# Kernel tuning notes

Measured on AMD Instinct MI355X. Metric: run time of the kernel, lower is better.

Reference implementation:

```python
import jax, jax.numpy as jnp
import numpy as np

N_DRUG = 20000
N_DIS = 20000
E = 300000
D_IN = 128
D_OUT = 128
W_SCALE = 0.05  # ~xavier-ish scale so leaky_relu/softmax stay well-conditioned


def setup_inputs() -> dict:
    key = jax.random.key(0)
    ks = jax.random.split(key, 17)
    f32 = jnp.float32
    inp = {
        'feat_drug': jax.random.normal(ks[0], (N_DRUG, D_IN), dtype=f32),
        'feat_disease': jax.random.normal(ks[1], (N_DIS, D_IN), dtype=f32),
        'W_ind': jax.random.normal(ks[2], (D_IN, D_OUT), dtype=f32) * W_SCALE,
        'b_ind': jax.random.normal(ks[3], (D_OUT,), dtype=f32) * W_SCALE,
        'a_ind': jax.random.normal(ks[4], (2 * D_OUT,), dtype=f32) * W_SCALE,
        'W_rev': jax.random.normal(ks[5], (D_IN, D_OUT), dtype=f32) * W_SCALE,
        'b_rev': jax.random.normal(ks[6], (D_OUT,), dtype=f32) * W_SCALE,
        'a_rev': jax.random.normal(ks[7], (2 * D_OUT,), dtype=f32) * W_SCALE,
        'W_dd': jax.random.normal(ks[8], (D_IN, D_OUT), dtype=f32) * W_SCALE,
        'b_dd': jax.random.normal(ks[9], (D_OUT,), dtype=f32) * W_SCALE,
        'a_dd': jax.random.normal(ks[10], (2 * D_OUT,), dtype=f32) * W_SCALE,
        'src_ind': jax.random.randint(ks[11], (E,), 0, N_DRUG, dtype=jnp.int32),
        'dst_ind': jax.random.randint(ks[12], (E,), 0, N_DIS, dtype=jnp.int32),
        'src_rev': jax.random.randint(ks[13], (E,), 0, N_DIS, dtype=jnp.int32),
        'dst_rev': jax.random.randint(ks[14], (E,), 0, N_DRUG, dtype=jnp.int32),
        'src_dd': jax.random.randint(ks[15], (E,), 0, N_DIS, dtype=jnp.int32),
        'dst_dd': jax.random.randint(ks[16], (E,), 0, N_DIS, dtype=jnp.int32),
    }
    return inp


def segment_softmax(e, seg, num_segments):
    # numerically stable softmax over variable-degree neighborhoods (dst segments)
    m = jax.ops.segment_max(e, seg, num_segments=num_segments)
    p = jnp.exp(e - m[seg])
    s = jax.ops.segment_sum(p, seg, num_segments=num_segments)
    return p / s[seg]


def _etype_agg(Wh_src, Wh_dst_key, a, src, dst, n_dst):
    # attn_fc(cat([Wh_src[src], Wh_dst_key[dst]])) decomposed into per-node
    # scalar projections, then gathered per edge (same math, far less traffic)
    d = Wh_src.shape[1]
    el = Wh_src @ a[:d]        # [n_src]
    er = Wh_dst_key @ a[d:]    # [n_dst]
    e = jax.nn.leaky_relu(el[src] + er[dst])          # [E], slope 0.01 as in torch
    alpha = segment_softmax(e, dst, n_dst)            # per-dst softmax (DGL mailbox)
    msg = alpha[:, None] * Wh_src[src]                # [E, d]
    return jax.ops.segment_sum(msg, dst, num_segments=n_dst)


def reference(feat_drug, feat_disease, W_ind, b_ind, a_ind, W_rev, b_rev, a_rev,
              W_dd, b_dd, a_dd, src_ind, dst_ind, src_rev, dst_rev, src_dd, dst_dd):
    # per-etype linear on source node type
    Wh_ind = feat_drug @ W_ind + b_ind       # drug nodes, etype 'indication'
    Wh_rev = feat_disease @ W_rev + b_rev    # disease nodes, etype 'rev_indication'
    Wh_dd = feat_disease @ W_dd + b_dd       # disease nodes, etype 'disease_disease'
    n_drug = feat_drug.shape[0]
    n_dis = feat_disease.shape[0]
    # etype 'indication' (drug->disease): dst key is Wh_rev_indication
    h_dis_ind = _etype_agg(Wh_ind, Wh_rev, a_ind, src_ind, dst_ind, n_dis)
    # etype 'rev_indication' (disease->drug): dst key is Wh_indication
    h_drug = _etype_agg(Wh_rev, Wh_ind, a_rev, src_rev, dst_rev, n_drug)
    # etype 'disease_disease' (homotypic): both keys Wh_dd
    h_dis_dd = _etype_agg(Wh_dd, Wh_dd, a_dd, src_dd, dst_dd, n_dis)
    # multi_update_all(..., 'sum'): sum per-etype reductions per dst node type
    h_disease = h_dis_ind + h_dis_dd
    return h_drug, h_disease
```

## Files before the change

### kernel.cpp

```cpp
#include <hip/hip_runtime.h>
#include <hip/hip_bf16.h>

typedef __hip_bfloat16 bf16;
typedef __attribute__((ext_vector_type(8))) short bf16x8;
typedef __attribute__((ext_vector_type(4))) float f32x4;

#define N_NODE 20000
#define D      128
#define NEDGE  300000
#define NROW   (3 * N_NODE)
#define NBIN   ((NROW + 255) >> 8)
#define NB3    220
#define CHUNK  4096
#define GBE    ((N_NODE + 63) / 64)
#define GEMMB  (3 * GBE)
#define WT_LD  132

__device__ __forceinline__ short f2bs(float x) {
    bf16 h = __float2bfloat16(x);
    short s; __builtin_memcpy(&s, &h, 2); return s;
}

union SharedA {
    short Wt[D * WT_LD];
    int   h[NBIN];
};

__global__ __launch_bounds__(256) void gemm_and_count(
    const float* __restrict__ feat_drug, const float* __restrict__ feat_dis,
    const float* __restrict__ W_ind, const float* __restrict__ b_ind,
    const float* __restrict__ a_ind,
    const float* __restrict__ W_rev, const float* __restrict__ b_rev,
    const float* __restrict__ a_rev,
    const float* __restrict__ W_dd, const float* __restrict__ b_dd,
    const float* __restrict__ a_dd,
    const int* __restrict__ dst_rev, const int* __restrict__ dst_ind,
    const int* __restrict__ dst_dd,
    bf16* __restrict__ Wh_all, float* __restrict__ el_all,
    float* __restrict__ er_all, int* __restrict__ bin_part) {
    __shared__ SharedA su;
    const int tid = threadIdx.x;

    if (blockIdx.x >= GEMMB) {
        const int blk = blockIdx.x - GEMMB;
        for (int i = tid; i < NBIN; i += 256) su.h[i] = 0;
        __syncthreads();
        const int base = blk * CHUNK;
        const int lim = min(base + CHUNK, 3 * NEDGE);
        for (int i = base + tid; i < lim; i += 256) {
            const int t = (i >= 2 * NEDGE) ? 2 : (i >= NEDGE ? 1 : 0);
            const int e = i - t * NEDGE;
            const int d = (t == 0 ? dst_rev : (t == 1 ? dst_ind : dst_dd))[e];
            atomicAdd(&su.h[(t * N_NODE + d) >> 8], 1);
        }
        __syncthreads();
        for (int i = tid; i < NBIN; i += 256)
            bin_part[blk * NBIN + i] = su.h[i];
        return;
    }

    const int t  = blockIdx.x / GBE;
    const int mb = blockIdx.x - t * GBE;

    const float *feat, *W, *bias, *va, *vb;
    float *el_o, *er_o;
    if (t == 0)      { feat = feat_dis;  W = W_rev; bias = b_rev; va = a_rev; vb = a_ind + D; el_o = el_all;              er_o = er_all + N_NODE; }
    else if (t == 1) { feat = feat_drug; W = W_ind; bias = b_ind; va = a_ind; vb = a_rev + D; el_o = el_all + N_NODE;     er_o = er_all; }
    else             { feat = feat_dis;  W = W_dd;  bias = b_dd;  va = a_dd;  vb = a_dd + D;  el_o = el_all + 2 * N_NODE; er_o = er_all + 2 * N_NODE; }
    bf16* wh_o = Wh_all + (size_t)t * N_NODE * D;

    for (int i = tid * 4; i < D * D; i += 1024) {
        const float4 wv = *(const float4*)(W + i);
        const int k = i >> 7, n = i & (D - 1);
        su.Wt[(n + 0) * WT_LD + k] = f2bs(wv.x);
        su.Wt[(n + 1) * WT_LD + k] = f2bs(wv.y);
        su.Wt[(n + 2) * WT_LD + k] = f2bs(wv.z);
        su.Wt[(n + 3) * WT_LD + k] = f2bs(wv.w);
    }
    __syncthreads();

    const int wave = tid >> 6, lane = tid & 63;
    const int q = lane >> 4, nn = lane & 15;
    const int row0 = mb * 64 + wave * 16;
    const int arow = min(row0 + nn, N_NODE - 1);

    f32x4 acc[8];
#pragma unroll
    for (int nt = 0; nt < 8; ++nt) acc[nt] = (f32x4){0.f, 0.f, 0.f, 0.f};

#pragma unroll
    for (int ks = 0; ks < 4; ++ks) {
        const float* ap = feat + (size_t)arow * D + ks * 32 + q * 8;
        const float4 fa = *(const float4*)ap;
        const float4 fb = *(const float4*)(ap + 4);
        bf16x8 afrag;
        afrag[0] = f2bs(fa.x); afrag[1] = f2bs(fa.y);
        afrag[2] = f2bs(fa.z); afrag[3] = f2bs(fa.w);
        afrag[4] = f2bs(fb.x); afrag[5] = f2bs(fb.y);
        afrag[6] = f2bs(fb.z); afrag[7] = f2bs(fb.w);
#pragma unroll
        for (int nt = 0; nt < 8; ++nt) {
            const bf16x8 bfrag =
                *(const bf16x8*)(&su.Wt[(nt * 16 + nn) * WT_LD + ks * 32 + q * 8]);
            acc[nt] = __builtin_amdgcn_mfma_f32_16x16x32_bf16(afrag, bfrag,
                                                              acc[nt], 0, 0, 0);
        }
    }

    float biasv[8], vav[8], vbv[8];
#pragma unroll
    for (int nt = 0; nt < 8; ++nt) {
        const int col = nt * 16 + nn;
        biasv[nt] = bias[col]; vav[nt] = va[col]; vbv[nt] = vb[col];
    }
    float pel[4] = {0.f, 0.f, 0.f, 0.f};
    float per_[4] = {0.f, 0.f, 0.f, 0.f};
    short* whs = (short*)wh_o;
#pragma unroll
    for (int nt = 0; nt < 8; ++nt) {
#pragma unroll
        for (int r = 0; r < 4; ++r) {
            const float c = acc[nt][r] + biasv[nt];
            const int grow = row0 + q * 4 + r;
            if (grow < N_NODE)
                whs[(size_t)grow * D + nt * 16 + nn] = f2bs(c);
            pel[r] = fmaf(c, vav[nt], pel[r]);
            per_[r] = fmaf(c, vbv[nt], per_[r]);
        }
    }
#pragma unroll
    for (int r = 0; r < 4; ++r) {
#pragma unroll
        for (int mask = 1; mask < 16; mask <<= 1) {
            pel[r]  += __shfl_xor(pel[r],  mask, 64);
            per_[r] += __shfl_xor(per_[r], mask, 64);
        }
        const int grow = row0 + q * 4 + r;
        if (nn == 0 && grow < N_NODE) {
            el_o[grow] = pel[r];
            er_o[grow] = per_[r];
        }
    }
}

__global__ __launch_bounds__(256) void binscat(
    const int* __restrict__ src_rev, const int* __restrict__ dst_rev,
    const int* __restrict__ src_ind, const int* __restrict__ dst_ind,
    const int* __restrict__ src_dd,  const int* __restrict__ dst_dd,
    const int* __restrict__ bin_part, int* __restrict__ bin_base_g,
    int* __restrict__ row_ptr, unsigned* __restrict__ bin_buf) {
    __shared__ int runc[NBIN];
    __shared__ int wsum[4];
    const int blk = blockIdx.x;
    const int tid = threadIdx.x;
    const int lane = tid & 63, wave = tid >> 6;

    int tot = 0, pre = 0;
    if (tid < NBIN) {
        for (int j = 0; j < NB3; ++j) {
            const int c = bin_part[j * NBIN + tid];
            tot += c;
            pre += (j < blk) ? c : 0;
        }
    }
    int v = (tid < NBIN) ? tot : 0;
    const int orig = v;
#pragma unroll
    for (int off = 1; off < 64; off <<= 1) {
        int t = __shfl_up(v, off, 64);
        if (lane >= off) v += t;
    }
    if (lane == 63) wsum[wave] = v;
    __syncthreads();
    if (tid == 0) {
        int a = 0;
#pragma unroll
        for (int w = 0; w < 4; ++w) { int t = wsum[w]; wsum[w] = a; a += t; }
    }
    __syncthreads();
    const int excl = wsum[wave] + v - orig;
    if (tid < NBIN) runc[tid] = excl + pre;
    if (blk == 0) {
        if (tid < NBIN) bin_base_g[tid] = excl;
        if (tid == 0) { bin_base_g[NBIN] = 3 * NEDGE; row_ptr[NROW] = 3 * NEDGE; }
    }
    __syncthreads();

    const int base = blk * CHUNK;
    const int lim = min(base + CHUNK, 3 * NEDGE);
    for (int i = base + tid; i < lim; i += 256) {
        const int t = (i >= 2 * NEDGE) ? 2 : (i >= NEDGE ? 1 : 0);
        const int e = i - t * NEDGE;
        const int sl = (t == 0 ? src_rev : (t == 1 ? src_ind : src_dd))[e];
        const int dl = (t == 0 ? dst_rev : (t == 1 ? dst_ind : dst_dd))[e];
        const int row = t * N_NODE + dl;
        const int slot = atomicAdd(&runc[row >> 8], 1);
        bin_buf[slot] = ((unsigned)row << 16) | (unsigned)(t * N_NODE + sl);
    }
}

__global__ __launch_bounds__(256) void binsort(
    const int* __restrict__ bin_base, const unsigned* __restrict__ bin_buf,
    int* __restrict__ row_ptr, unsigned short* __restrict__ edge_src16) {
    __shared__ int rowcnt[256];
    __shared__ int rankc[256];
    __shared__ int wsum[4];
    const int b = blockIdx.x;
    const int tid = threadIdx.x;
    const int beg = bin_base[b], end = bin_base[b + 1];
    rowcnt[tid] = 0;
    __syncthreads();
    for (int i = beg + tid; i < end; i += 256)
        atomicAdd(&rowcnt[(bin_buf[i] >> 16) & 255], 1);
    __syncthreads();
    const int lane = tid & 63, wave = tid >> 6;
    int v = rowcnt[tid];
    const int orig = v;
#pragma unroll
    for (int off = 1; off < 64; off <<= 1) {
        int t = __shfl_up(v, off, 64);
        if (lane >= off) v += t;
    }
    if (lane == 63) wsum[wave] = v;
    __syncthreads();
    if (tid == 0) {
        int a = 0;
#pragma unroll
        for (int w = 0; w < 4; ++w) { int t = wsum[w]; wsum[w] = a; a += t; }
    }
    __syncthreads();
    const int excl = wsum[wave] + v - orig;
    const int row = b * 256 + tid;
    if (row < NROW) row_ptr[row] = beg + excl;
    rankc[tid] = beg + excl;
    __syncthreads();
    for (int i = beg + tid; i < end; i += 256) {
        const unsigned u = bin_buf[i];
        const int slot = atomicAdd(&rankc[(u >> 16) & 255], 1);
        edge_src16[slot] = (unsigned short)(u & 0xFFFFu);
    }
}

__device__ __forceinline__ void process_chunk(
    int msrc, float mpe, int m, float inv, int sub, int fl,
    const bf16* __restrict__ Wh_all, float* __restrict__ acc) {
#pragma unroll 2
    for (int t = 0; t < m; t += 4) {
        const int   s = __shfl(msrc, t + sub, 64);
        const float c = __shfl(mpe,  t + sub, 64) * inv;
        const uint4 u = ((const uint4*)(Wh_all + (size_t)s * D))[fl];
        acc[0] = fmaf(c, __uint_as_float(u.x << 16),          acc[0]);
        acc[1] = fmaf(c, __uint_as_float(u.x & 0xFFFF0000u),  acc[1]);
        acc[2] = fmaf(c, __uint_as_float(u.y << 16),          acc[2]);
        acc[3] = fmaf(c, __uint_as_float(u.y & 0xFFFF0000u),  acc[3]);
        acc[4] = fmaf(c, __uint_as_float(u.z << 16),          acc[4]);
        acc[5] = fmaf(c, __uint_as_float(u.z & 0xFFFF0000u),  acc[5]);
        acc[6] = fmaf(c, __uint_as_float(u.w << 16),          acc[6]);
        acc[7] = fmaf(c, __uint_as_float(u.w & 0xFFFF0000u),  acc[7]);
    }
}

__device__ __forceinline__ void do_range(
    const unsigned short* __restrict__ edge_src16,
    const float* __restrict__ el_all, float er_r,
    const bf16* __restrict__ Wh_all,
    int beg, int end, int lane, int sub, int fl, float* __restrict__ acc) {
    if (end <= beg) return;
    const int deg = end - beg;
    const int m0 = min(deg, 64);

    int msrc0 = 0; float mpe0 = 0.f;
    if (lane < m0) {
        msrc0 = edge_src16[beg + lane];
        float v = el_all[msrc0] + er_r;
        v = v > 0.f ? v : 0.01f * v;
        mpe0 = __expf(v);
    }
    float ssum = mpe0;
    for (int base = beg + 64; base < end; base += 64) {
        const int m = min(end - base, 64);
        if (lane < m) {
            const int sr = edge_src16[base + lane];
            float v = el_all[sr] + er_r;
            v = v > 0.f ? v : 0.01f * v;
            ssum += __expf(v);
        }
    }
#pragma unroll
    for (int off = 32; off > 0; off >>= 1) ssum += __shfl_down(ssum, off, 64);
    const float inv = 1.0f / __shfl(ssum, 0, 64);

    process_chunk(msrc0, mpe0, m0, inv, sub, fl, Wh_all, acc);
    for (int base = beg + 64; base < end; base += 64) {
        const int m = min(end - base, 64);
        int msrc = 0; float mpe = 0.f;
        if (lane < m) {
            msrc = edge_src16[base + lane];
            float v = el_all[msrc] + er_r;
            v = v > 0.f ? v : 0.01f * v;
            mpe = __expf(v);
        }
        process_chunk(msrc, mpe, m, inv, sub, fl, Wh_all, acc);
    }
}

__global__ __launch_bounds__(256) void gather_all(
    const int* __restrict__ row_ptr, const unsigned short* __restrict__ edge_src16,
    const float* __restrict__ el_all, const float* __restrict__ er_all,
    const bf16* __restrict__ Wh_all, float* __restrict__ out) {
    const int w = blockIdx.x * (blockDim.x >> 6) + (threadIdx.x >> 6);
    const int lane = threadIdx.x & 63;
    if (w >= 2 * N_NODE) return;
    const int sub = lane >> 4, fl = lane & 15;

    float acc[8];
#pragma unroll
    for (int j = 0; j < 8; ++j) acc[j] = 0.f;

    do_range(edge_src16, el_all, er_all[w], Wh_all,
             row_ptr[w], row_ptr[w + 1], lane, sub, fl, acc);
    if (w >= N_NODE) {
        const int r = w + N_NODE;
        do_range(edge_src16, el_all, er_all[r], Wh_all,
                 row_ptr[r], row_ptr[r + 1], lane, sub, fl, acc);
    }

#pragma unroll
    for (int j = 0; j < 8; ++j) {
        acc[j] += __shfl_xor(acc[j], 16, 64);
        acc[j] += __shfl_xor(acc[j], 32, 64);
    }
    if (sub == 0) {
        float4* orow = (float4*)(out + (size_t)w * D);
        orow[2 * fl]     = make_float4(acc[0], acc[1], acc[2], acc[3]);
        orow[2 * fl + 1] = make_float4(acc[4], acc[5], acc[6], acc[7]);
    }
}

extern "C" void kernel_launch(void* const* d_in, const int* in_sizes, int n_in,
                              void* d_out, int out_size, void* d_ws, size_t ws_size,
                              hipStream_t stream) {
    const float* feat_drug    = (const float*)d_in[0];
    const float* feat_disease = (const float*)d_in[1];
    const float* W_ind = (const float*)d_in[2];
    const float* b_ind = (const float*)d_in[3];
    const float* a_ind = (const float*)d_in[4];
    const float* W_rev = (const float*)d_in[5];
    const float* b_rev = (const float*)d_in[6];
    const float* a_rev = (const float*)d_in[7];
    const float* W_dd  = (const float*)d_in[8];
    const float* b_dd  = (const float*)d_in[9];
    const float* a_dd  = (const float*)d_in[10];
    const int* src_ind = (const int*)d_in[11];
    const int* dst_ind = (const int*)d_in[12];
    const int* src_rev = (const int*)d_in[13];
    const int* dst_rev = (const int*)d_in[14];
    const int* src_dd  = (const int*)d_in[15];
    const int* dst_dd  = (const int*)d_in[16];
    float* out = (float*)d_out;
    (void)in_sizes; (void)n_in; (void)out_size; (void)ws_size;

    char* w = (char*)d_ws;
    bf16*  Wh_all   = (bf16*)w;
    float* el_all   = (float*)(w + 15360000);
    float* er_all   = (float*)(w + 15600000);
    int*   row_ptr  = (int*)(w + 15840000);
    int*   bin_base = (int*)(w + 16080032);
    int*   bin_part = (int*)(w + 16081056);
    unsigned* bin_buf = (unsigned*)(w + 16287872);
    unsigned short* edge_src16 = (unsigned short*)(w + 19887872);

    const int gb = (2 * N_NODE + 3) / 4;

    gemm_and_count<<<GEMMB + NB3, 256, 0, stream>>>(
        feat_drug, feat_disease, W_ind, b_ind, a_ind,
        W_rev, b_rev, a_rev, W_dd, b_dd, a_dd,
        dst_rev, dst_ind, dst_dd, Wh_all, el_all, er_all, bin_part);

    binscat<<<NB3, 256, 0, stream>>>(src_rev, dst_rev, src_ind, dst_ind,
                                     src_dd, dst_dd, bin_part, bin_base,
                                     row_ptr, bin_buf);

    binsort<<<NBIN, 256, 0, stream>>>(bin_base, bin_buf, row_ptr, edge_src16);

    gather_all<<<gb, 256, 0, stream>>>(row_ptr, edge_src16, el_all, er_all,
                                       Wh_all, out);
}
```

Measured before the change: 183.1 us.

## Fuse bin count, scatter and sort into GEMM kernel with grid barriers

Merges the binscat and binsort kernels into the GEMM+count kernel. The NBIN binning blocks coordinate through two global atomic spin barriers, so one launch does count, prefix, scatter and per-bin sort. This removes two kernel launches and their drain/fill gaps, and lets the binning work overlap with the GEMM blocks. The cost is that spin barriers require all NBIN blocks to be co-resident. If GEMM blocks are scheduled first, binning blocks may wait, and an extra memset launch is added to reset the barrier counters.

Result: slower. 272.1 us (+48.6%).

```diff
diff --git a/kernel.cpp b/kernel.cpp
--- a/kernel.cpp
+++ b/kernel.cpp
@@ -10,8 +10,7 @@
 #define NEDGE  300000
 #define NROW   (3 * N_NODE)
 #define NBIN   ((NROW + 255) >> 8)
-#define NB3    220
-#define CHUNK  4096
+#define CHUNK3 ((3 * NEDGE + NBIN - 1) / NBIN)
 #define GBE    ((N_NODE + 63) / 64)
 #define GEMMB  (3 * GBE)
 #define WT_LD  132
@@ -21,12 +20,31 @@
     short s; __builtin_memcpy(&s, &h, 2); return s;
 }
 
+__device__ __forceinline__ void bin_barrier(int* bar, int target) {
+    __syncthreads();
+    if (threadIdx.x == 0) {
+        __threadfence();
+        atomicAdd(bar, 1);
+        while (__hip_atomic_load(bar, __ATOMIC_ACQUIRE,
+                                 __HIP_MEMORY_SCOPE_AGENT) < target)
+            __builtin_amdgcn_s_sleep(8);
+    }
+    __syncthreads();
+    __threadfence();
+}
+
 union SharedA {
     short Wt[D * WT_LD];
-    int   h[NBIN];
+    struct {
+        int cnt[NBIN];
+        int sbase[NBIN + 1];
+        int wsum[4];
+        int rowcnt[256];
+        int rankc[256];
+    } b;
 };
 
-__global__ __launch_bounds__(256) void gemm_and_count(
+__global__ __launch_bounds__(256) void gemm_and_bins(
     const float* __restrict__ feat_drug, const float* __restrict__ feat_dis,
     const float* __restrict__ W_ind, const float* __restrict__ b_ind,
     const float* __restrict__ a_ind,
@@ -34,28 +52,108 @@
     const float* __restrict__ a_rev,
     const float* __restrict__ W_dd, const float* __restrict__ b_dd,
     const float* __restrict__ a_dd,
-    const int* __restrict__ dst_rev, const int* __restrict__ dst_ind,
-    const int* __restrict__ dst_dd,
+    const int* __restrict__ src_rev, const int* __restrict__ dst_rev,
+    const int* __restrict__ src_ind, const int* __restrict__ dst_ind,
+    const int* __restrict__ src_dd,  const int* __restrict__ dst_dd,
     bf16* __restrict__ Wh_all, float* __restrict__ el_all,
-    float* __restrict__ er_all, int* __restrict__ bin_part) {
+    float* __restrict__ er_all, int* __restrict__ bin_part,
+    unsigned* __restrict__ bin_buf, int* __restrict__ row_ptr,
+    unsigned short* __restrict__ edge_src16, int* __restrict__ bar) {
     __shared__ SharedA su;
     const int tid = threadIdx.x;
 
     if (blockIdx.x >= GEMMB) {
         const int blk = blockIdx.x - GEMMB;
-        for (int i = tid; i < NBIN; i += 256) su.h[i] = 0;
-        __syncthreads();
-        const int base = blk * CHUNK;
-        const int lim = min(base + CHUNK, 3 * NEDGE);
+        const int lane = tid & 63, wave = tid >> 6;
+
+        for (int i = tid; i < NBIN; i += 256) su.b.cnt[i] = 0;
+        __syncthreads();
+        const int base = blk * CHUNK3;
+        const int lim = min(base + CHUNK3, 3 * NEDGE);
         for (int i = base + tid; i < lim; i += 256) {
             const int t = (i >= 2 * NEDGE) ? 2 : (i >= NEDGE ? 1 : 0);
             const int e = i - t * NEDGE;
             const int d = (t == 0 ? dst_rev : (t == 1 ? dst_ind : dst_dd))[e];
-            atomicAdd(&su.h[(t * N_NODE + d) >> 8], 1);
+            atomicAdd(&su.b.cnt[(t * N_NODE + d) >> 8], 1);
         }
         __syncthreads();
         for (int i = tid; i < NBIN; i += 256)
-            bin_part[blk * NBIN + i] = su.h[i];
+            bin_part[blk * NBIN + i] = su.b.cnt[i];
+        bin_barrier(bar + 0, NBIN);
+
+        int tot = 0, pre = 0;
+        if (tid < NBIN) {
+            for (int j = 0; j < NBIN; ++j) {
+                const int c = bin_part[j * NBIN + tid];
+                tot += c;
+                pre += (j < blk) ? c : 0;
+            }
+        }
+        int v = (tid < NBIN) ? tot : 0;
+        const int orig = v;
+#pragma unroll
+        for (int off = 1; off < 64; off <<= 1) {
+            int t = __shfl_up(v, off, 64);
+            if (lane >= off) v += t;
+        }
+        if (lane == 63) su.b.wsum[wave] = v;
+        __syncthreads();
+        if (tid == 0) {
+            int a = 0;
+#pragma unroll
+            for (int w = 0; w < 4; ++w) { int t = su.b.wsum[w]; su.b.wsum[w] = a; a += t; }
+        }
+        __syncthreads();
+        const int excl = su.b.wsum[wave] + v - orig;
+        if (tid < NBIN) {
+            su.b.sbase[tid] = excl;
+            su.b.cnt[tid] = excl + pre;
+        }
+        if (tid == 0) su.b.sbase[NBIN] = 3 * NEDGE;
+        if (blk == 0 && tid == 0) row_ptr[NROW] = 3 * NEDGE;
+        __syncthreads();
+        for (int i = base + tid; i < lim; i += 256) {
+            const int t = (i >= 2 * NEDGE) ? 2 : (i >= NEDGE ? 1 : 0);
+            const int e = i - t * NEDGE;
+            const int sl = (t == 0 ? src_rev : (t == 1 ? src_ind : src_dd))[e];
+            const int dl = (t == 0 ? dst_rev : (t == 1 ? dst_ind : dst_dd))[e];
+            const int row = t * N_NODE + dl;
+            const int slot = atomicAdd(&su.b.cnt[row >> 8], 1);
+            bin_buf[slot] = ((unsigned)row << 16) | (unsigned)(t * N_NODE + sl);
+        }
+        bin_barrier(bar + 1, NBIN);
+
+        const int beg = su.b.sbase[blk], end = su.b.sbase[blk + 1];
+        su.b.rowcnt[tid] = 0;
+        __syncthreads();
+        for (int i = beg + tid; i < end; i += 256)
+            atomicAdd(&su.b.rowcnt[(bin_buf[i] >> 16) & 255], 1);
+        __syncthreads();
+        int v3 = su.b.rowcnt[tid];
+        const int orig3 = v3;
+#pragma unroll
+        for (int off = 1; off < 64; off <<= 1) {
+            int t = __shfl_up(v3, off, 64);
+            if (lane >= off) v3 += t;
+        }
+        if (lane == 63) su.b.wsum[wave] = v3;
+        __syncthreads();
+        if (tid == 0) {
+            int a = 0;
+#pragma unroll
+            for (int w = 0; w < 4; ++w) { int t = su.b.wsum[w]; su.b.wsum[w] = a; a += t; }
+        }
+        __syncthreads();
+        const int excl3 = su.b.wsum[wave] + v3 - orig3;
+        const int row = blk * 256 + tid;
+        if (row < NROW) row_ptr[row] = beg + excl3;
+        su.b.rankc[tid] = beg + excl3;
+        __syncthreads();
+        for (int i = beg + tid; i < end; i += 256) {
+            const unsigned u = bin_buf[i];
+            const int slot = atomicAdd(&su.b.rankc[(u >> 16) & 255], 1);
+            edge_src16[slot] = (unsigned short)(u & 0xFFFFu);
+        }
         return;
     }
 
@@ -140,104 +238,6 @@
             el_o[grow] = pel[r];
             er_o[grow] = per_[r];
         }
-    }
-}
-
-__global__ __launch_bounds__(256) void binscat(
-    const int* __restrict__ src_rev, const int* __restrict__ dst_rev,
-    const int* __restrict__ src_ind, const int* __restrict__ dst_ind,
-    const int* __restrict__ src_dd,  const int* __restrict__ dst_dd,
-    const int* __restrict__ bin_part, int* __restrict__ bin_base_g,
-    int* __restrict__ row_ptr, unsigned* __restrict__ bin_buf) {
-    __shared__ int runc[NBIN];
-    __shared__ int wsum[4];
-    const int blk = blockIdx.x;
-    const int tid = threadIdx.x;
-    const int lane = tid & 63, wave = tid >> 6;
-
-    int tot = 0, pre = 0;
-    if (tid < NBIN) {
-        for (int j = 0; j < NB3; ++j) {
-            const int c = bin_part[j * NBIN + tid];
-            tot += c;
-            pre += (j < blk) ? c : 0;
-        }
-    }
-    int v = (tid < NBIN) ? tot : 0;
-    const int orig = v;
-#pragma unroll
-    for (int off = 1; off < 64; off <<= 1) {
-        int t = __shfl_up(v, off, 64);
-        if (lane >= off) v += t;
-    }
-    if (lane == 63) wsum[wave] = v;
-    __syncthreads();
-    if (tid == 0) {
-        int a = 0;
-#pragma unroll
-        for (int w = 0; w < 4; ++w) { int t = wsum[w]; wsum[w] = a; a += t; }
-    }
-    __syncthreads();
-    const int excl = wsum[wave] + v - orig;
-    if (tid < NBIN) runc[tid] = excl + pre;
-    if (blk == 0) {
-        if (tid < NBIN) bin_base_g[tid] = excl;
-        if (tid == 0) { bin_base_g[NBIN] = 3 * NEDGE; row_ptr[NROW] = 3 * NEDGE; }
-    }
-    __syncthreads();
-
-    const int base = blk * CHUNK;
-    const int lim = min(base + CHUNK, 3 * NEDGE);
-    for (int i = base + tid; i < lim; i += 256) {
-        const int t = (i >= 2 * NEDGE) ? 2 : (i >= NEDGE ? 1 : 0);
-        const int e = i - t * NEDGE;
-        const int sl = (t == 0 ? src_rev : (t == 1 ? src_ind : src_dd))[e];
-        const int dl = (t == 0 ? dst_rev : (t == 1 ? dst_ind : dst_dd))[e];
-        const int row = t * N_NODE + dl;
-        const int slot = atomicAdd(&runc[row >> 8], 1);
-        bin_buf[slot] = ((unsigned)row << 16) | (unsigned)(t * N_NODE + sl);
-    }
-}
-
-__global__ __launch_bounds__(256) void binsort(
-    const int* __restrict__ bin_base, const unsigned* __restrict__ bin_buf,
-    int* __restrict__ row_ptr, unsigned short* __restrict__ edge_src16) {
-    __shared__ int rowcnt[256];
-    __shared__ int rankc[256];
-    __shared__ int wsum[4];
-    const int b = blockIdx.x;
-    const int tid = threadIdx.x;
-    const int beg = bin_base[b], end = bin_base[b + 1];
-    rowcnt[tid] = 0;
-    __syncthreads();
-    for (int i = beg + tid; i < end; i += 256)
-        atomicAdd(&rowcnt[(bin_buf[i] >> 16) & 255], 1);
-    __syncthreads();
-    const int lane = tid & 63, wave = tid >> 6;
-    int v = rowcnt[tid];
-    const int orig = v;
-#pragma unroll
-    for (int off = 1; off < 64; off <<= 1) {
-        int t = __shfl_up(v, off, 64);
-        if (lane >= off) v += t;
-    }
-    if (lane == 63) wsum[wave] = v;
-    __syncthreads();
-    if (tid == 0) {
-        int a = 0;
-#pragma unroll
-        for (int w = 0; w < 4; ++w) { int t = wsum[w]; wsum[w] = a; a += t; }
-    }
-    __syncthreads();
-    const int excl = wsum[wave] + v - orig;
-    const int row = b * 256 + tid;
-    if (row < NROW) row_ptr[row] = beg + excl;
-    rankc[tid] = beg + excl;
-    __syncthreads();
-    for (int i = beg + tid; i < end; i += 256) {
-        const unsigned u = bin_buf[i];
-        const int slot = atomicAdd(&rankc[(u >> 16) & 255], 1);
-        edge_src16[slot] = (unsigned short)(u & 0xFFFFu);
     }
 }
 
@@ -365,23 +365,20 @@
     float* el_all   = (float*)(w + 15360000);
     float* er_all   = (float*)(w + 15600000);
     int*   row_ptr  = (int*)(w + 15840000);
-    int*   bin_base = (int*)(w + 16080032);
-    int*   bin_part = (int*)(w + 16081056);
-    unsigned* bin_buf = (unsigned*)(w + 16287872);
-    unsigned short* edge_src16 = (unsigned short*)(w + 19887872);
+    int*   bar      = (int*)(w + 16080032);
+    int*   bin_part = (int*)(w + 16080064);
+    unsigned* bin_buf = (unsigned*)(w + 16300992);
+    unsigned short* edge_src16 = (unsigned short*)(w + 19900992);
 
     const int gb = (2 * N_NODE + 3) / 4;
 
-    gemm_and_count<<<GEMMB + NB3, 256, 0, stream>>>(
+    hipMemsetAsync(bar, 0, 2 * sizeof(int), stream);
+
+    gemm_and_bins<<<GEMMB + NBIN, 256, 0, stream>>>(
         feat_drug, feat_disease, W_ind, b_ind, a_ind,
         W_rev, b_rev, a_rev, W_dd, b_dd, a_dd,
-        dst_rev, dst_ind, dst_dd, Wh_all, el_all, er_all, bin_part);
-
-    binscat<<<NB3, 256, 0, stream>>>(src_rev, dst_rev, src_ind, dst_ind,
-                                     src_dd, dst_dd, bin_part, bin_base,
-                                     row_ptr, bin_buf);
-
-    binsort<<<NBIN, 256, 0, stream>>>(bin_base, bin_buf, row_ptr, edge_src16);
+        src_rev, dst_rev, src_ind, dst_ind, src_dd, dst_dd,
+        Wh_all, el_all, er_all, bin_part, bin_buf, row_ptr, edge_src16, bar);
 
     gather_all<<<gb, 256, 0, stream>>>(row_ptr, edge_src16, el_all, er_all,
                                        Wh_all, out);
```
